# Kernel tuning notes

Hardware: AMD Instinct MI355X
Metric: run time of the kernel (lower is better)

The kernel has to match this reference:

```python
import jax, jax.numpy as jnp
import numpy as np

B = 1048576
H = 32
DAMP_MIN = jnp.array([0.001, 0.001], dtype=jnp.float32)

def setup_inputs() -> dict:
    key = jax.random.key(0)
    ks = jax.random.split(key, 13)
    u = lambda k, shape: jax.random.uniform(k, shape, jnp.float32, -0.2, 0.2)
    return {
        "x": jax.random.normal(ks[0], (B, 2), jnp.float32),
        "w_d1": u(ks[1], (2, H)),
        "w_d2": u(ks[2], (H, H)),
        "w_d3": u(ks[3], (H, 2)),
        "w_o1": u(ks[4], (2, H)),
        "w_o2": u(ks[5], (H, H)),
        "w_o3": u(ks[6], (H, 1)),
        "b_d1": jnp.zeros((H,), jnp.float32),
        "b_d2": jnp.zeros((H,), jnp.float32),
        "b_d3": jnp.zeros((2,), jnp.float32),
        "b_o1": jnp.zeros((H,), jnp.float32),
        "b_o2": jnp.zeros((H,), jnp.float32),
        "b_o3": jnp.zeros((1,), jnp.float32),
    }

def reference(x, w_d1, w_d2, w_d3, w_o1, w_o2, w_o3,
              b_d1, b_d2, b_d3, b_o1, b_o2, b_o3):
    # diag branch: 2-layer tanh MLP -> relu, scaled by x
    d1t = jnp.tanh(x @ w_d1 + b_d1)
    d2t = jnp.tanh(d1t @ w_d2 + b_d2)
    d3 = d2t @ w_d3 + b_d3                       # [B,2]
    d3r = (jax.nn.relu(d3) + DAMP_MIN) * x       # diag of L, [B,2]
    # off-diag branch -> single lower-triangular element per sample
    o1t = jnp.tanh(x @ w_o1 + b_o1)
    o2t = jnp.tanh(o1t @ w_o2 + b_o2)
    o3 = o2t @ w_o3 + b_o3                       # [B,1]
    # L = [[a,0],[c,b]] per sample; D = (L L^T) x, vectorized over batch.
    a = d3r[:, 0]
    b = d3r[:, 1]
    c = o3[:, 0]
    x0 = x[:, 0]
    x1 = x[:, 1]
    D0 = a * a * x0 + a * c * x1
    D1 = a * c * x0 + (c * c + b * b) * x1
    return jnp.stack([D0, D1], axis=-1)          # [B,2]
```

## Files before the change

kernel.cpp:

```cpp
#include <hip/hip_runtime.h>


typedef __bf16 bf16x8 __attribute__((ext_vector_type(8)));
typedef float f32x4 __attribute__((ext_vector_type(4)));
typedef int i32x4 __attribute__((ext_vector_type(4)));

#define TANH_SCALE 2.8853900817779268f

__device__ __forceinline__ float fast_tanh_pre(float y) {
    float e = __builtin_amdgcn_exp2f(y);
    float r = __builtin_amdgcn_rcpf(e + 1.0f);
    return __builtin_fmaf(-2.0f, r, 1.0f);
}

__device__ __forceinline__ int pack_bf16(float f0, float f1) {
    unsigned u0 = __builtin_bit_cast(unsigned, f0) + 0x8000u;
    unsigned u1 = __builtin_bit_cast(unsigned, f1) + 0x8000u;
    return (int)__builtin_amdgcn_perm(u1, u0, 0x07060302u);
}

__global__ __launch_bounds__(256, 4) void damping_mfma(
    const float* __restrict__ x,
    const float* __restrict__ w_d1, const float* __restrict__ w_d2, const float* __restrict__ w_d3,
    const float* __restrict__ w_o1, const float* __restrict__ w_o2, const float* __restrict__ w_o3,
    const float* __restrict__ b_d1, const float* __restrict__ b_d2, const float* __restrict__ b_d3,
    const float* __restrict__ b_o1, const float* __restrict__ b_o2, const float* __restrict__ b_o3,
    float* __restrict__ out, int n_tiles)
{
    const int lane = threadIdx.x & 63;
    const int quad = lane >> 4;
    const int b16  = lane & 15;
    const int wid     = (int)((blockIdx.x * blockDim.x + threadIdx.x) >> 6);
    const int n_waves = (int)((gridDim.x * blockDim.x) >> 6);

    float w1d0[8], w1d1[8], bd1[8], w1o0[8], w1o1[8], bo1[8];
    #pragma unroll
    for (int j = 0; j < 8; ++j) {
        int k = quad * 8 + j;
        w1d0[j] = w_d1[k] * TANH_SCALE; w1d1[j] = w_d1[32 + k] * TANH_SCALE;
        bd1[j]  = b_d1[k] * TANH_SCALE;
        w1o0[j] = w_o1[k] * TANH_SCALE; w1o1[j] = w_o1[32 + k] * TANH_SCALE;
        bo1[j]  = b_o1[k] * TANH_SCALE;
    }
    bf16x8 a_d2[2], a_o2[2];
    #pragma unroll
    for (int t = 0; t < 2; ++t) {
        #pragma unroll
        for (int j = 0; j < 8; ++j) {
            int k = quad * 8 + j;
            a_d2[t][j] = (__bf16)(w_d2[k * 32 + t * 16 + b16] * TANH_SCALE);
            a_o2[t][j] = (__bf16)(w_o2[k * 32 + t * 16 + b16] * TANH_SCALE);
        }
    }
    float bd2[8], bo2[8], w3d0[8], w3d1[8], w3o[8];
    #pragma unroll
    for (int i = 0; i < 8; ++i) {
        int jj = (i >> 2) * 16 + quad * 4 + (i & 3);
        bd2[i]  = b_d2[jj] * TANH_SCALE; bo2[i] = b_o2[jj] * TANH_SCALE;
        w3d0[i] = w_d3[jj * 2]; w3d1[i] = w_d3[jj * 2 + 1];
        w3o[i]  = w_o3[jj];
    }
    const float bd3_0 = b_d3[0], bd3_1 = b_d3[1], bo3_0 = b_o3[0];

    const float2* x2 = (const float2*)x;

    for (int tile = wid; tile < n_tiles; tile += n_waves) {
        float2 xv = x2[tile * 16 + b16];
        const float x0 = xv.x, x1 = xv.y;

        float hd[8], ho[8];
        #pragma unroll
        for (int j = 0; j < 8; ++j) {
            hd[j] = fast_tanh_pre(fmaf(x1, w1d1[j], fmaf(x0, w1d0[j], bd1[j])));
            ho[j] = fast_tanh_pre(fmaf(x1, w1o1[j], fmaf(x0, w1o0[j], bo1[j])));
        }
        i32x4 pd_, po_;
        #pragma unroll
        for (int p = 0; p < 4; ++p) {
            pd_[p] = pack_bf16(hd[2 * p], hd[2 * p + 1]);
            po_[p] = pack_bf16(ho[2 * p], ho[2 * p + 1]);
        }
        bf16x8 bfd = __builtin_bit_cast(bf16x8, pd_);
        bf16x8 bfo = __builtin_bit_cast(bf16x8, po_);

        f32x4 zero = {0.f, 0.f, 0.f, 0.f};
        f32x4 d0 = __builtin_amdgcn_mfma_f32_16x16x32_bf16(a_d2[0], bfd, zero, 0, 0, 0);
        f32x4 d1 = __builtin_amdgcn_mfma_f32_16x16x32_bf16(a_d2[1], bfd, zero, 0, 0, 0);
        f32x4 o0 = __builtin_amdgcn_mfma_f32_16x16x32_bf16(a_o2[0], bfo, zero, 0, 0, 0);
        f32x4 o1 = __builtin_amdgcn_mfma_f32_16x16x32_bf16(a_o2[1], bfo, zero, 0, 0, 0);

        float pd0 = 0.f, pd1 = 0.f, po = 0.f;
        #pragma unroll
        for (int i = 0; i < 8; ++i) {
            float vd = (i < 4 ? d0[i] : d1[i - 4]) + bd2[i];
            float vo = (i < 4 ? o0[i] : o1[i - 4]) + bo2[i];
            float h2d = fast_tanh_pre(vd);
            float h2o = fast_tanh_pre(vo);
            pd0 = fmaf(h2d, w3d0[i], pd0);
            pd1 = fmaf(h2d, w3d1[i], pd1);
            po  = fmaf(h2o, w3o[i], po);
        }
        pd0 += __shfl_xor(pd0, 16); pd0 += __shfl_xor(pd0, 32);
        pd1 += __shfl_xor(pd1, 16); pd1 += __shfl_xor(pd1, 32);
        po  += __shfl_xor(po, 16);  po  += __shfl_xor(po, 32);

        float d30 = pd0 + bd3_0, d31 = pd1 + bd3_1, c = po + bo3_0;
        float a = (fmaxf(d30, 0.f) + 0.001f) * x0;
        float b = (fmaxf(d31, 0.f) + 0.001f) * x1;
        float D0 = fmaf(a * a, x0, a * c * x1);
        float D1 = fmaf(a * c, x0, fmaf(c, c, b * b) * x1);

        if (quad == 0) ((float2*)out)[tile * 16 + b16] = make_float2(D0, D1);
    }
}

extern "C" void kernel_launch(void* const* d_in, const int* in_sizes, int n_in,
                              void* d_out, int out_size, void* d_ws, size_t ws_size,
                              hipStream_t stream) {
    const float* x    = (const float*)d_in[0];
    const float* w_d1 = (const float*)d_in[1];
    const float* w_d2 = (const float*)d_in[2];
    const float* w_d3 = (const float*)d_in[3];
    const float* w_o1 = (const float*)d_in[4];
    const float* w_o2 = (const float*)d_in[5];
    const float* w_o3 = (const float*)d_in[6];
    const float* b_d1 = (const float*)d_in[7];
    const float* b_d2 = (const float*)d_in[8];
    const float* b_d3 = (const float*)d_in[9];
    const float* b_o1 = (const float*)d_in[10];
    const float* b_o2 = (const float*)d_in[11];
    const float* b_o3 = (const float*)d_in[12];
    float* out = (float*)d_out;

    int n = in_sizes[0] / 2;
    int n_tiles = n / 16;
    int blocks_needed = (n_tiles + 3) / 4;
    int grid = blocks_needed < 1792 ? blocks_needed : 1792;
    damping_mfma<<<grid, 256, 0, stream>>>(
        x, w_d1, w_d2, w_d3, w_o1, w_o2, w_o3,
        b_d1, b_d2, b_d3, b_o1, b_o2, b_o3, out, n_tiles);
}
```

Measured before the change: 127.5 us.

## Replace transcendental tanh with packed fp16 polynomial tanh and fp16 MFMA

Replaces the exp2/rcp-based fp32 tanh with a packed half2 tanh. It builds exp2 by exponent-bit construction plus a cubic polynomial and computes the reciprocal with Newton iterations, so every instruction processes two values using packed fp16 ALU ops instead of per-element transcendental-unit ops. The MFMA input changes from bf16 to fp16 to match the packed outputs. This trades the transcendental-unit throughput bottleneck for more packed ALU instructions and lower precision, adding conversion overhead in the second layer.

Result: slower. 138.7 us (+8.8%).

```diff
diff --git a/kernel.cpp b/kernel.cpp
--- a/kernel.cpp
+++ b/kernel.cpp
@@ -1,22 +1,41 @@
 #include <hip/hip_runtime.h>
 
 
-typedef __bf16 bf16x8 __attribute__((ext_vector_type(8)));
-typedef float f32x4 __attribute__((ext_vector_type(4)));
-typedef int i32x4 __attribute__((ext_vector_type(4)));
+typedef _Float16 h2   __attribute__((ext_vector_type(2)));
+typedef _Float16 h8   __attribute__((ext_vector_type(8)));
+typedef float    f32x4 __attribute__((ext_vector_type(4)));
+typedef unsigned u32x4 __attribute__((ext_vector_type(4)));
 
 #define TANH_SCALE 2.8853900817779268f
 
-__device__ __forceinline__ float fast_tanh_pre(float y) {
-    float e = __builtin_amdgcn_exp2f(y);
-    float r = __builtin_amdgcn_rcpf(e + 1.0f);
-    return __builtin_fmaf(-2.0f, r, 1.0f);
+__device__ __forceinline__ h2 h2s(float x) { _Float16 v = (_Float16)x; h2 r = {v, v}; return r; }
+
+__device__ __forceinline__ h2 pk(float a, float b) {
+    return __builtin_bit_cast(h2, __builtin_amdgcn_cvt_pkrtz(a, b));
 }
 
-__device__ __forceinline__ int pack_bf16(float f0, float f1) {
-    unsigned u0 = __builtin_bit_cast(unsigned, f0) + 0x8000u;
-    unsigned u1 = __builtin_bit_cast(unsigned, f1) + 0x8000u;
-    return (int)__builtin_amdgcn_perm(u1, u0, 0x07060302u);
+__device__ __forceinline__ h2 tanh2pk(h2 yh) {
+    const h2 one = h2s(1.0f), two = h2s(2.0f);
+    unsigned yb  = __builtin_bit_cast(unsigned, yh);
+    unsigned sgn = yb & 0x80008000u;
+    h2 ay = __builtin_bit_cast(h2, yb & 0x7FFF7FFFu);
+    h2 v  = __builtin_elementwise_min(ay, h2s(15.0f));
+    h2 Y  = v + h2s(1536.0f);
+    h2 k  = Y - h2s(1536.0f);
+    h2 g  = k - v;
+    unsigned Sb = (0x660F660Fu - __builtin_bit_cast(unsigned, Y)) << 10;
+    h2 S = __builtin_bit_cast(h2, Sb);
+    h2 p = __builtin_elementwise_fma(g,
+             __builtin_elementwise_fma(g,
+               __builtin_elementwise_fma(g, h2s(0.0555041f), h2s(0.2402265f)),
+               h2s(0.6931472f)), one);
+    h2 E = S * p;
+    h2 z = E + one;
+    h2 r = __builtin_elementwise_fma(E, h2s(-0.5f), one);
+    r = r * __builtin_elementwise_fma(-z, r, two);
+    r = r * __builtin_elementwise_fma(-z, r, two);
+    h2 th = __builtin_elementwise_fma(two, r, h2s(-1.0f));
+    return __builtin_bit_cast(h2, __builtin_bit_cast(unsigned, th) | sgn);
 }
 
 __global__ __launch_bounds__(256, 4) void damping_mfma(
@@ -42,14 +61,14 @@
         w1o0[j] = w_o1[k] * TANH_SCALE; w1o1[j] = w_o1[32 + k] * TANH_SCALE;
         bo1[j]  = b_o1[k] * TANH_SCALE;
     }
-    bf16x8 a_d2[2], a_o2[2];
+    h8 a_d2[2], a_o2[2];
     #pragma unroll
     for (int t = 0; t < 2; ++t) {
         #pragma unroll
         for (int j = 0; j < 8; ++j) {
             int k = quad * 8 + j;
-            a_d2[t][j] = (__bf16)(w_d2[k * 32 + t * 16 + b16] * TANH_SCALE);
-            a_o2[t][j] = (__bf16)(w_o2[k * 32 + t * 16 + b16] * TANH_SCALE);
+            a_d2[t][j] = (_Float16)(w_d2[k * 32 + t * 16 + b16] * TANH_SCALE);
+            a_o2[t][j] = (_Float16)(w_o2[k * 32 + t * 16 + b16] * TANH_SCALE);
         }
     }
     float bd2[8], bo2[8], w3d0[8], w3d1[8], w3o[8];
@@ -68,37 +87,38 @@
         float2 xv = x2[tile * 16 + b16];
         const float x0 = xv.x, x1 = xv.y;
 
-        float hd[8], ho[8];
-        #pragma unroll
-        for (int j = 0; j < 8; ++j) {
-            hd[j] = fast_tanh_pre(fmaf(x1, w1d1[j], fmaf(x0, w1d0[j], bd1[j])));
-            ho[j] = fast_tanh_pre(fmaf(x1, w1o1[j], fmaf(x0, w1o0[j], bo1[j])));
-        }
-        i32x4 pd_, po_;
+        u32x4 bd_, bo_;
         #pragma unroll
         for (int p = 0; p < 4; ++p) {
-            pd_[p] = pack_bf16(hd[2 * p], hd[2 * p + 1]);
-            po_[p] = pack_bf16(ho[2 * p], ho[2 * p + 1]);
+            float pd0 = fmaf(x1, w1d1[2*p],   fmaf(x0, w1d0[2*p],   bd1[2*p]));
+            float pd1 = fmaf(x1, w1d1[2*p+1], fmaf(x0, w1d0[2*p+1], bd1[2*p+1]));
+            float po0 = fmaf(x1, w1o1[2*p],   fmaf(x0, w1o0[2*p],   bo1[2*p]));
+            float po1 = fmaf(x1, w1o1[2*p+1], fmaf(x0, w1o0[2*p+1], bo1[2*p+1]));
+            bd_[p] = __builtin_bit_cast(unsigned, tanh2pk(pk(pd0, pd1)));
+            bo_[p] = __builtin_bit_cast(unsigned, tanh2pk(pk(po0, po1)));
         }
-        bf16x8 bfd = __builtin_bit_cast(bf16x8, pd_);
-        bf16x8 bfo = __builtin_bit_cast(bf16x8, po_);
+        h8 Bd = __builtin_bit_cast(h8, bd_);
+        h8 Bo = __builtin_bit_cast(h8, bo_);
 
         f32x4 zero = {0.f, 0.f, 0.f, 0.f};
-        f32x4 d0 = __builtin_amdgcn_mfma_f32_16x16x32_bf16(a_d2[0], bfd, zero, 0, 0, 0);
-        f32x4 d1 = __builtin_amdgcn_mfma_f32_16x16x32_bf16(a_d2[1], bfd, zero, 0, 0, 0);
-        f32x4 o0 = __builtin_amdgcn_mfma_f32_16x16x32_bf16(a_o2[0], bfo, zero, 0, 0, 0);
-        f32x4 o1 = __builtin_amdgcn_mfma_f32_16x16x32_bf16(a_o2[1], bfo, zero, 0, 0, 0);
+        f32x4 d0 = __builtin_amdgcn_mfma_f32_16x16x32_f16(a_d2[0], Bd, zero, 0, 0, 0);
+        f32x4 d1 = __builtin_amdgcn_mfma_f32_16x16x32_f16(a_d2[1], Bd, zero, 0, 0, 0);
+        f32x4 o0 = __builtin_amdgcn_mfma_f32_16x16x32_f16(a_o2[0], Bo, zero, 0, 0, 0);
+        f32x4 o1 = __builtin_amdgcn_mfma_f32_16x16x32_f16(a_o2[1], Bo, zero, 0, 0, 0);
 
         float pd0 = 0.f, pd1 = 0.f, po = 0.f;
         #pragma unroll
-        for (int i = 0; i < 8; ++i) {
-            float vd = (i < 4 ? d0[i] : d1[i - 4]) + bd2[i];
-            float vo = (i < 4 ? o0[i] : o1[i - 4]) + bo2[i];
-            float h2d = fast_tanh_pre(vd);
-            float h2o = fast_tanh_pre(vo);
-            pd0 = fmaf(h2d, w3d0[i], pd0);
-            pd1 = fmaf(h2d, w3d1[i], pd1);
-            po  = fmaf(h2o, w3o[i], po);
+        for (int p = 0; p < 4; ++p) {
+            int i0 = 2 * p, i1 = 2 * p + 1;
+            float vd0 = (i0 < 4 ? d0[i0] : d1[i0 - 4]) + bd2[i0];
+            float vd1 = (i1 < 4 ? d0[i1] : d1[i1 - 4]) + bd2[i1];
+            float vo0 = (i0 < 4 ? o0[i0] : o1[i0 - 4]) + bo2[i0];
+            float vo1 = (i1 < 4 ? o0[i1] : o1[i1 - 4]) + bo2[i1];
+            h2 td = tanh2pk(pk(vd0, vd1));
+            h2 to = tanh2pk(pk(vo0, vo1));
+            pd0 = fmaf((float)td[0], w3d0[i0], fmaf((float)td[1], w3d0[i1], pd0));
+            pd1 = fmaf((float)td[0], w3d1[i0], fmaf((float)td[1], w3d1[i1], pd1));
+            po  = fmaf((float)to[0], w3o[i0],  fmaf((float)to[1], w3o[i1],  po));
         }
         pd0 += __shfl_xor(pd0, 16); pd0 += __shfl_xor(pd0, 32);
         pd1 += __shfl_xor(pd1, 16); pd1 += __shfl_xor(pd1, 32);
```
